# Kernel tuning notes

Hardware: AMD Instinct MI355X
Metric: run time of the kernel (lower is better)

The kernel has to match this reference:

```python
import jax, jax.numpy as jnp
import numpy as np

D_MODEL = 768
NUM_HEADS = 12
D_HEAD = D_MODEL // NUM_HEADS


def setup_inputs() -> dict:
    key = jax.random.key(0)
    ks = jax.random.split(key, 11)
    B, S = 2, 2048
    scale = 1.0 / np.sqrt(D_MODEL)
    inp = {
        "query": jax.random.normal(ks[0], (B, S, D_MODEL), dtype=jnp.float32),
        "key": jax.random.normal(ks[1], (B, S, D_MODEL), dtype=jnp.float32),
        "value": jax.random.normal(ks[2], (B, S, D_MODEL), dtype=jnp.float32),
        "W_q": jax.random.normal(ks[3], (D_MODEL, D_MODEL), dtype=jnp.float32) * scale,
        "b_q": jnp.zeros((D_MODEL,), dtype=jnp.float32),
        "W_k": jax.random.normal(ks[4], (D_MODEL, D_MODEL), dtype=jnp.float32) * scale,
        "b_k": jnp.zeros((D_MODEL,), dtype=jnp.float32),
        "W_v": jax.random.normal(ks[5], (D_MODEL, D_MODEL), dtype=jnp.float32) * scale,
        "b_v": jnp.zeros((D_MODEL,), dtype=jnp.float32),
        "W_o": jax.random.normal(ks[6], (D_MODEL, D_MODEL), dtype=jnp.float32) * scale,
        "b_o": jnp.zeros((D_MODEL,), dtype=jnp.float32),
    }
    return inp


def _split_heads(x):
    # [B, S, D] -> [B, H, S, Dh]
    B, S, _ = x.shape
    return x.reshape(B, S, NUM_HEADS, D_HEAD).transpose(0, 2, 1, 3)


def reference(query, key, value, W_q, b_q, W_k, b_k, W_v, b_v, W_o, b_o):
    q = _split_heads(query @ W_q.T + b_q)   # [B,H,S,Dh]
    k = _split_heads(key @ W_k.T + b_k)
    v = _split_heads(value @ W_v.T + b_v)
    scores = jnp.einsum('bhqd,bhkd->bhqk', q, k) / np.sqrt(D_HEAD).astype(np.float32)
    attn = jax.nn.softmax(scores, axis=-1)  # [B,H,S,S]
    out = jnp.einsum('bhqk,bhkd->bhqd', attn, v)
    B, H, S, Dh = out.shape
    out = out.transpose(0, 2, 1, 3).reshape(B, S, D_MODEL)
    out = out @ W_o.T + b_o
    return out, attn
```

## Files before the change

### kernel.cpp

```cpp
#include <hip/hip_runtime.h>
#include <hip/hip_bf16.h>
#include <stdint.h>

#define B_ 2
#define S_ 2048
#define D_ 768
#define H_ 12
#define DH_ 64
#define M_ (B_ * S_)

typedef __hip_bfloat16 bf16_t;
typedef __attribute__((ext_vector_type(8))) short bf16x8;
typedef __attribute__((ext_vector_type(4))) float f32x4;

__device__ __forceinline__ void async_cp16(const void* g, void* lds) {
  __builtin_amdgcn_global_load_lds(
      (__attribute__((address_space(1))) void*)g,
      (__attribute__((address_space(3))) void*)lds, 16, 0, 0);
}

__global__ __launch_bounds__(256) void cvt_kernel(
    const float* __restrict__ s0, const float* __restrict__ s1,
    const float* __restrict__ s2, const float* __restrict__ s3,
    const float* __restrict__ s4, const float* __restrict__ s5,
    const float* __restrict__ s6,
    bf16_t* __restrict__ d0, bf16_t* __restrict__ d1, bf16_t* __restrict__ d2,
    bf16_t* __restrict__ d3, bf16_t* __restrict__ d4, bf16_t* __restrict__ d5,
    bf16_t* __restrict__ d6) {
  const int NX = 786432;
  const int NW = 147456;
  int idx = blockIdx.x * 256 + threadIdx.x;
  const float* s; bf16_t* d; int l;
  if      (idx < NX)            { s = s0; d = d0; l = idx; }
  else if (idx < 2 * NX)        { s = s1; d = d1; l = idx - NX; }
  else if (idx < 3 * NX)        { s = s2; d = d2; l = idx - 2 * NX; }
  else if (idx < 3 * NX + NW)   { s = s3; d = d3; l = idx - 3 * NX; }
  else if (idx < 3 * NX + 2*NW) { s = s4; d = d4; l = idx - (3 * NX + NW); }
  else if (idx < 3 * NX + 3*NW) { s = s5; d = d5; l = idx - (3 * NX + 2 * NW); }
  else                          { s = s6; d = d6; l = idx - (3 * NX + 3 * NW); }
  float4 f = ((const float4*)s)[l];
  union { bf16_t h[4]; uint64_t u; } pk;
  pk.h[0] = __float2bfloat16(f.x); pk.h[1] = __float2bfloat16(f.y);
  pk.h[2] = __float2bfloat16(f.z); pk.h[3] = __float2bfloat16(f.w);
  ((uint64_t*)d)[l] = pk.u;
}

__device__ __forceinline__ void gemm_core(
    const bf16_t* __restrict__ A, const bf16_t* __restrict__ W,
    bf16_t* sA, bf16_t* sB, int m0, int n0, f32x4 acc[4][4]) {
  const int tid = threadIdx.x;
  const int wave = tid >> 6, lane = tid & 63;
  const int quad = lane >> 4, col = lane & 15;
  const int wm = wave >> 1, wn = wave & 1;

  for (int kt = 0; kt < 768; kt += 64) {
    __syncthreads();
#pragma unroll
    for (int r2 = 0; r2 < 4; ++r2) {
      int cbase = r2 * 256 + wave * 64;
      int c = cbase + lane;
      int row = c >> 3, cpos = c & 7, csrc = cpos ^ (row & 7);
      async_cp16(A + (size_t)(m0 + row) * 768 + kt + csrc * 8, (char*)sA + cbase * 16);
      async_cp16(W + (size_t)(n0 + row) * 768 + kt + csrc * 8, (char*)sB + cbase * 16);
    }
    __syncthreads();
#pragma unroll
    for (int ks = 0; ks < 2; ++ks) {
      const int cl = ks * 4 + quad;
      bf16x8 af[4], bf8[4];
#pragma unroll
      for (int i = 0; i < 4; ++i) {
        int m = wm * 64 + i * 16 + col;
        af[i] = *(const bf16x8*)((const char*)sA + m * 128 + ((cl ^ (m & 7)) * 16));
      }
#pragma unroll
      for (int j = 0; j < 4; ++j) {
        int n = wn * 64 + j * 16 + col;
        bf8[j] = *(const bf16x8*)((const char*)sB + n * 128 + ((cl ^ (n & 7)) * 16));
      }
#pragma unroll
      for (int i = 0; i < 4; ++i)
#pragma unroll
        for (int j = 0; j < 4; ++j)
          acc[i][j] = __builtin_amdgcn_mfma_f32_16x16x32_bf16(af[i], bf8[j], acc[i][j], 0, 0, 0);
    }
  }
}

__global__ __launch_bounds__(256, 2) void qkv_gemm_kernel(
    const bf16_t* __restrict__ xq, const bf16_t* __restrict__ xk, const bf16_t* __restrict__ xv,
    const bf16_t* __restrict__ wq, const bf16_t* __restrict__ wk, const bf16_t* __restrict__ wv,
    const float* __restrict__ bq, const float* __restrict__ bk, const float* __restrict__ bv,
    bf16_t* __restrict__ Qb, bf16_t* __restrict__ Kb, bf16_t* __restrict__ Vt) {
  __shared__ bf16_t sA[128 * 64];
  __shared__ bf16_t sB[128 * 64];
  const int z = blockIdx.z;
  const bf16_t* A = (z == 0) ? xq : (z == 1) ? xk : xv;
  const bf16_t* W = (z == 0) ? wq : (z == 1) ? wk : wv;
  const float* bias = (z == 0) ? bq : (z == 1) ? bk : bv;
  const int m0 = blockIdx.y * 128, n0 = blockIdx.x * 128;
  f32x4 acc[4][4] = {};
  gemm_core(A, W, sA, sB, m0, n0, acc);

  const int tid = threadIdx.x;
  const int wave = tid >> 6, lane = tid & 63;
  const int quad = lane >> 4, col = lane & 15;
  const int wm = wave >> 1, wn = wave & 1;
  float bv4[4];
#pragma unroll
  for (int j = 0; j < 4; ++j) bv4[j] = bias[n0 + wn * 64 + j * 16 + col];

  if (z == 2) {
#pragma unroll
    for (int i = 0; i < 4; ++i)
#pragma unroll
      for (int j = 0; j < 4; ++j) {
        union { bf16_t h[4]; uint64_t u; } pk;
#pragma unroll
        for (int r = 0; r < 4; ++r) pk.h[r] = __float2bfloat16(acc[i][j][r] + bv4[j]);
        int sbase = m0 + wm * 64 + i * 16 + quad * 4;
        int b = sbase >> 11, s = sbase & 2047;
        int ng = n0 + wn * 64 + j * 16 + col;
        int h = ng >> 6, d = ng & 63;
        *(uint64_t*)(Vt + (((size_t)(b * H_ + h)) * DH_ + d) * S_ + s) = pk.u;
      }
  } else {
    const float scale = (z == 0) ? 0.125f : 1.0f;
    bf16_t* dst = (z == 0) ? Qb : Kb;
#pragma unroll
    for (int i = 0; i < 4; ++i)
#pragma unroll
      for (int j = 0; j < 4; ++j)
#pragma unroll
        for (int r = 0; r < 4; ++r) {
          int mg = m0 + wm * 64 + i * 16 + quad * 4 + r;
          int ng = n0 + wn * 64 + j * 16 + col;
          int b = mg >> 11, s = mg & 2047;
          int h = ng >> 6, d = ng & 63;
          dst[(((size_t)(b * H_ + h)) * S_ + s) * DH_ + d] =
              __float2bfloat16((acc[i][j][r] + bv4[j]) * scale);
        }
  }
}

__global__ __launch_bounds__(256, 2) void o_gemm_kernel(
    const bf16_t* __restrict__ Ob, const bf16_t* __restrict__ wo,
    const float* __restrict__ bo, float* __restrict__ out) {
  __shared__ bf16_t sA[128 * 64];
  __shared__ bf16_t sB[128 * 64];
  const int m0 = blockIdx.y * 128, n0 = blockIdx.x * 128;
  f32x4 acc[4][4] = {};
  gemm_core(Ob, wo, sA, sB, m0, n0, acc);
  const int tid = threadIdx.x;
  const int wave = tid >> 6, lane = tid & 63;
  const int quad = lane >> 4, col = lane & 15;
  const int wm = wave >> 1, wn = wave & 1;
  float bv4[4];
#pragma unroll
  for (int j = 0; j < 4; ++j) bv4[j] = bo[n0 + wn * 64 + j * 16 + col];
#pragma unroll
  for (int i = 0; i < 4; ++i)
#pragma unroll
    for (int j = 0; j < 4; ++j)
#pragma unroll
      for (int r = 0; r < 4; ++r) {
        int mg = m0 + wm * 64 + i * 16 + quad * 4 + r;
        int ng = n0 + wn * 64 + j * 16 + col;
        out[(size_t)mg * D_ + ng] = acc[i][j][r] + bv4[j];
      }
}

__global__ __launch_bounds__(256, 3) void attn_kernel(
    const bf16_t* __restrict__ Qb, const bf16_t* __restrict__ Kb,
    const bf16_t* __restrict__ Vt, float* __restrict__ attn,
    bf16_t* __restrict__ Ob) {
  __shared__ bf16_t sP[2][64 * 128];
  __shared__ float red[4][64];

  const int tid = threadIdx.x;
  const int w = tid >> 6, lane = tid & 63;
  const int quad = lane >> 4, col = lane & 15;
  const int qt = blockIdx.x, bh = blockIdx.y;
  const int bb = bh / H_, hh = bh - bb * H_;
  const size_t headSD = (size_t)bh * (S_ * DH_);
  const size_t headDS = (size_t)bh * (DH_ * S_);
  const int q0 = qt * 64;

  bf16x8 aq[2][4];
#pragma unroll
  for (int ks = 0; ks < 2; ++ks)
#pragma unroll
    for (int i = 0; i < 4; ++i)
      aq[ks][i] = *(const bf16x8*)(Qb + headSD +
                    (size_t)(q0 + i * 16 + col) * DH_ + ks * 32 + quad * 8);

  float rsum[4][4] = {};
  for (int t = 0; t < 16; ++t) {
    const int k0 = t * 128 + w * 32;
    bf16x8 bk[2][2];
#pragma unroll
    for (int ks = 0; ks < 2; ++ks)
#pragma unroll
      for (int j = 0; j < 2; ++j)
        bk[ks][j] = *(const bf16x8*)(Kb + headSD +
                      (size_t)(k0 + j * 16 + col) * DH_ + ks * 32 + quad * 8);
    f32x4 sc[4][2] = {};
#pragma unroll
    for (int ks = 0; ks < 2; ++ks)
#pragma unroll
      for (int i = 0; i < 4; ++i)
#pragma unroll
        for (int j = 0; j < 2; ++j)
          sc[i][j] = __builtin_amdgcn_mfma_f32_16x16x32_bf16(aq[ks][i], bk[ks][j], sc[i][j], 0, 0, 0);
#pragma unroll
    for (int i = 0; i < 4; ++i)
#pragma unroll
      for (int r = 0; r < 4; ++r)
        rsum[i][r] += __expf(sc[i][0][r]) + __expf(sc[i][1][r]);
  }
#pragma unroll
  for (int d = 1; d < 16; d <<= 1)
#pragma unroll
    for (int i = 0; i < 4; ++i)
#pragma unroll
      for (int r = 0; r < 4; ++r)
        rsum[i][r] += __shfl_xor(rsum[i][r], d, 64);
  if (col == 0) {
#pragma unroll
    for (int i = 0; i < 4; ++i)
#pragma unroll
      for (int r = 0; r < 4; ++r)
        red[w][i * 16 + quad * 4 + r] = rsum[i][r];
  }
  __syncthreads();
  float li[4][4];
#pragma unroll
  for (int i = 0; i < 4; ++i)
#pragma unroll
    for (int r = 0; r < 4; ++r) {
      int q = i * 16 + quad * 4 + r;
      li[i][r] = 1.0f / (red[0][q] + red[1][q] + red[2][q] + red[3][q]);
    }

  f32x4 oacc[4] = {};
  for (int t = 0; t < 16; ++t) {
    const int k0 = t * 128 + w * 32;
    bf16x8 bk[2][2];
#pragma unroll
    for (int ks = 0; ks < 2; ++ks)
#pragma unroll
      for (int j = 0; j < 2; ++j)
        bk[ks][j] = *(const bf16x8*)(Kb + headSD +
                      (size_t)(k0 + j * 16 + col) * DH_ + ks * 32 + quad * 8);
    f32x4 sc[4][2] = {};
#pragma unroll
    for (int ks = 0; ks < 2; ++ks)
#pragma unroll
      for (int i = 0; i < 4; ++i)
#pragma unroll
        for (int j = 0; j < 2; ++j)
          sc[i][j] = __builtin_amdgcn_mfma_f32_16x16x32_bf16(aq[ks][i], bk[ks][j], sc[i][j], 0, 0, 0);

    bf16_t* P = sP[t & 1];
#pragma unroll
    for (int i = 0; i < 4; ++i)
#pragma unroll
      for (int r = 0; r < 4; ++r) {
        int q = i * 16 + quad * 4 + r;
        float l = li[i][r];
        float* ap = attn + ((size_t)bh * S_ + (q0 + q)) * S_ + t * 128 + w * 32;
#pragma unroll
        for (int j = 0; j < 2; ++j) {
          float pa = __expf(sc[i][j][r]) * l;
          ap[j * 16 + col] = pa;
          int kk = w * 32 + j * 16 + col;
          int sch = (kk >> 3) ^ (q & 15);
          P[q * 128 + sch * 8 + (kk & 7)] = __float2bfloat16(pa);
        }
      }
    __syncthreads();
#pragma unroll
    for (int ksl = 0; ksl < 4; ++ksl) {
      int m = w * 16 + col;
      int sch = (ksl * 4 + quad) ^ (m & 15);
      bf16x8 ap8 = *(const bf16x8*)(P + m * 128 + sch * 8);
      bf16x8 bv[4];
#pragma unroll
      for (int j = 0; j < 4; ++j)
        bv[j] = *(const bf16x8*)(Vt + headDS + (size_t)(col + 16 * j) * S_ +
                                 t * 128 + ksl * 32 + quad * 8);
#pragma unroll
      for (int j = 0; j < 4; ++j)
        oacc[j] = __builtin_amdgcn_mfma_f32_16x16x32_bf16(ap8, bv[j], oacc[j], 0, 0, 0);
    }
  }

#pragma unroll
  for (int j = 0; j < 4; ++j)
#pragma unroll
    for (int r = 0; r < 4; ++r) {
      int q = q0 + w * 16 + quad * 4 + r;
      Ob[((size_t)bb * S_ + q) * D_ + hh * 64 + j * 16 + col] =
          __float2bfloat16(oacc[j][r]);
    }
}

extern "C" void kernel_launch(void* const* d_in, const int* in_sizes, int n_in,
                              void* d_out, int out_size, void* d_ws, size_t ws_size,
                              hipStream_t stream) {
  const float* q  = (const float*)d_in[0];
  const float* k  = (const float*)d_in[1];
  const float* v  = (const float*)d_in[2];
  const float* Wq = (const float*)d_in[3];
  const float* bq = (const float*)d_in[4];
  const float* Wk = (const float*)d_in[5];
  const float* bk = (const float*)d_in[6];
  const float* Wv = (const float*)d_in[7];
  const float* bv = (const float*)d_in[8];
  const float* Wo = (const float*)d_in[9];
  const float* bo = (const float*)d_in[10];
  char* ws = (char*)d_ws;
  bf16_t* xq = (bf16_t*)(ws + 0);
  bf16_t* xk = (bf16_t*)(ws + 6291456);
  bf16_t* xv = (bf16_t*)(ws + 12582912);
  bf16_t* wq = (bf16_t*)(ws + 18874368);
  bf16_t* wk = (bf16_t*)(ws + 20054016);
  bf16_t* wv = (bf16_t*)(ws + 21233664);
  bf16_t* wo = (bf16_t*)(ws + 22413312);
  bf16_t* Qb = (bf16_t*)(ws + 23592960);
  bf16_t* Kb = (bf16_t*)(ws + 29884416);
  bf16_t* Vt = (bf16_t*)(ws + 36175872);
  bf16_t* Ob = (bf16_t*)(ws + 42467328);
  float* out = (float*)d_out;
  float* attn = out + (size_t)M_ * D_;

  cvt_kernel<<<11520, 256, 0, stream>>>(q, k, v, Wq, Wk, Wv, Wo,
                                        xq, xk, xv, wq, wk, wv, wo);
  qkv_gemm_kernel<<<dim3(6, 32, 3), 256, 0, stream>>>(xq, xk, xv, wq, wk, wv,
                                                      bq, bk, bv, Qb, Kb, Vt);
  attn_kernel<<<dim3(32, 24), 256, 0, stream>>>(Qb, Kb, Vt, attn, Ob);
  o_gemm_kernel<<<dim3(6, 32), 256, 0, stream>>>(Ob, wo, bo, out);
}
```

Baseline: 618.1 us.

## Restructure attention so each wave owns 16 query rows, dropping LDS and barriers

Each wave now handles its own 16 query rows across all 2048 keys, where before the four waves split the key range of a 64-row tile. The QK^T product is computed transposed (K as the A operand), so each lane holds four consecutive key columns and the attention matrix is written as float4 vectors. The P fragment for the PV MFMA is rebuilt through cross-lane shuffles rather than an LDS staging buffer, which removes the shared memory, the row-sum reduction through LDS and all __syncthreads. The cost is that every wave now loads the full K and V streams for its head independently (more global/L2 traffic per block), and a loop of 64 short iterations replaces 16 longer ones.

```diff
diff --git a/kernel.cpp b/kernel.cpp
--- a/kernel.cpp
+++ b/kernel.cpp
@@ -174,9 +174,6 @@
     const bf16_t* __restrict__ Qb, const bf16_t* __restrict__ Kb,
     const bf16_t* __restrict__ Vt, float* __restrict__ attn,
     bf16_t* __restrict__ Ob) {
-  __shared__ bf16_t sP[2][64 * 128];
-  __shared__ float red[4][64];
-
   const int tid = threadIdx.x;
   const int w = tid >> 6, lane = tid & 63;
   const int quad = lane >> 4, col = lane & 15;
@@ -184,125 +181,112 @@
   const int bb = bh / H_, hh = bh - bb * H_;
   const size_t headSD = (size_t)bh * (S_ * DH_);
   const size_t headDS = (size_t)bh * (DH_ * S_);
-  const int q0 = qt * 64;
-
-  bf16x8 aq[2][4];
+  const int q0 = qt * 64 + w * 16;
+
+  bf16x8 aq[2];
 #pragma unroll
   for (int ks = 0; ks < 2; ++ks)
-#pragma unroll
-    for (int i = 0; i < 4; ++i)
-      aq[ks][i] = *(const bf16x8*)(Qb + headSD +
-                    (size_t)(q0 + i * 16 + col) * DH_ + ks * 32 + quad * 8);
-
-  float rsum[4][4] = {};
-  for (int t = 0; t < 16; ++t) {
-    const int k0 = t * 128 + w * 32;
+    aq[ks] = *(const bf16x8*)(Qb + headSD +
+                  (size_t)(q0 + col) * DH_ + ks * 32 + quad * 8);
+
+  float rsum = 0.f;
+  for (int t = 0; t < 64; ++t) {
+    const int kg = t * 32;
     bf16x8 bk[2][2];
 #pragma unroll
-    for (int ks = 0; ks < 2; ++ks)
-#pragma unroll
-      for (int j = 0; j < 2; ++j)
-        bk[ks][j] = *(const bf16x8*)(Kb + headSD +
-                      (size_t)(k0 + j * 16 + col) * DH_ + ks * 32 + quad * 8);
-    f32x4 sc[4][2] = {};
-#pragma unroll
-    for (int ks = 0; ks < 2; ++ks)
-#pragma unroll
-      for (int i = 0; i < 4; ++i)
-#pragma unroll
-        for (int j = 0; j < 2; ++j)
-          sc[i][j] = __builtin_amdgcn_mfma_f32_16x16x32_bf16(aq[ks][i], bk[ks][j], sc[i][j], 0, 0, 0);
-#pragma unroll
-    for (int i = 0; i < 4; ++i)
+    for (int kk = 0; kk < 2; ++kk)
+#pragma unroll
+      for (int ks = 0; ks < 2; ++ks)
+        bk[kk][ks] = *(const bf16x8*)(Kb + headSD +
+                        (size_t)(kg + kk * 16 + col) * DH_ + ks * 32 + quad * 8);
+    f32x4 sc[2] = {};
+#pragma unroll
+    for (int kk = 0; kk < 2; ++kk)
+#pragma unroll
+      for (int ks = 0; ks < 2; ++ks)
+        sc[kk] = __builtin_amdgcn_mfma_f32_16x16x32_bf16(bk[kk][ks], aq[ks], sc[kk], 0, 0, 0);
+#pragma unroll
+    for (int kk = 0; kk < 2; ++kk)
 #pragma unroll
       for (int r = 0; r < 4; ++r)
-        rsum[i][r] += __expf(sc[i][0][r]) + __expf(sc[i][1][r]);
+        rsum += __expf(sc[kk][r]);
   }
-#pragma unroll
-  for (int d = 1; d < 16; d <<= 1)
-#pragma unroll
-    for (int i = 0; i < 4; ++i)
+  rsum += __shfl_xor(rsum, 16, 64);
+  rsum += __shfl_xor(rsum, 32, 64);
+  const float li = 1.0f / rsum;
+
+  f32x4 oacc[4] = {};
+  float* aprow = attn + ((size_t)bh * S_ + (q0 + col)) * S_ + quad * 4;
+  for (int t = 0; t < 64; ++t) {
+    const int kg = t * 32;
+    bf16x8 bk[2][2];
+#pragma unroll
+    for (int kk = 0; kk < 2; ++kk)
+#pragma unroll
+      for (int ks = 0; ks < 2; ++ks)
+        bk[kk][ks] = *(const bf16x8*)(Kb + headSD +
+                        (size_t)(kg + kk * 16 + col) * DH_ + ks * 32 + quad * 8);
+    f32x4 sc[2] = {};
+#pragma unroll
+    for (int kk = 0; kk < 2; ++kk)
+#pragma unroll
+      for (int ks = 0; ks < 2; ++ks)
+        sc[kk] = __builtin_amdgcn_mfma_f32_16x16x32_bf16(bk[kk][ks], aq[ks], sc[kk], 0, 0, 0);
+
+    float pa[2][4];
+#pragma unroll
+    for (int kk = 0; kk < 2; ++kk)
 #pragma unroll
       for (int r = 0; r < 4; ++r)
-        rsum[i][r] += __shfl_xor(rsum[i][r], d, 64);
-  if (col == 0) {
-#pragma unroll
-    for (int i = 0; i < 4; ++i)
-#pragma unroll
-      for (int r = 0; r < 4; ++r)
-        red[w][i * 16 + quad * 4 + r] = rsum[i][r];
+        pa[kk][r] = __expf(sc[kk][r]) * li;
+
+    *(f32x4*)(aprow + kg)      = (f32x4){pa[0][0], pa[0][1], pa[0][2], pa[0][3]};
+    *(f32x4*)(aprow + kg + 16) = (f32x4){pa[1][0], pa[1][1], pa[1][2], pa[1][3]};
+
+    uint32_t dw[2][2];
+#pragma unroll
+    for (int kk = 0; kk < 2; ++kk)
+#pragma unroll
+      for (int p = 0; p < 2; ++p) {
+        union { bf16_t h[2]; uint32_t u; } pk2;
+        pk2.h[0] = __float2bfloat16(pa[kk][2 * p]);
+        pk2.h[1] = __float2bfloat16(pa[kk][2 * p + 1]);
+        dw[kk][p] = pk2.u;
+      }
+
+    const int s0 = ((2 * quad) & 3) * 16 + col;
+    const int s1 = ((2 * quad + 1) & 3) * 16 + col;
+    uint32_t a00 = (uint32_t)__shfl((int)dw[0][0], s0);
+    uint32_t a01 = (uint32_t)__shfl((int)dw[0][1], s0);
+    uint32_t a10 = (uint32_t)__shfl((int)dw[1][0], s0);
+    uint32_t a11 = (uint32_t)__shfl((int)dw[1][1], s0);
+    uint32_t b00 = (uint32_t)__shfl((int)dw[0][0], s1);
+    uint32_t b01 = (uint32_t)__shfl((int)dw[0][1], s1);
+    uint32_t b10 = (uint32_t)__shfl((int)dw[1][0], s1);
+    uint32_t b11 = (uint32_t)__shfl((int)dw[1][1], s1);
+    const bool hi2 = quad >= 2;
+    union { uint32_t u[4]; bf16x8 v; } fr;
+    fr.u[0] = hi2 ? a10 : a00;
+    fr.u[1] = hi2 ? a11 : a01;
+    fr.u[2] = hi2 ? b10 : b00;
+    fr.u[3] = hi2 ? b11 : b01;
+
+    bf16x8 bv[4];
+#pragma unroll
+    for (int j = 0; j < 4; ++j)
+      bv[j] = *(const bf16x8*)(Vt + headDS +
+                  (size_t)(16 * j + col) * S_ + kg + quad * 8);
+#pragma unroll
+    for (int j = 0; j < 4; ++j)
+      oacc[j] = __builtin_amdgcn_mfma_f32_16x16x32_bf16(fr.v, bv[j], oacc[j], 0, 0, 0);
   }
-  __syncthreads();
-  float li[4][4];
-#pragma unroll
-  for (int i = 0; i < 4; ++i)
-#pragma unroll
-    for (int r = 0; r < 4; ++r) {
-      int q = i * 16 + quad * 4 + r;
-      li[i][r] = 1.0f / (red[0][q] + red[1][q] + red[2][q] + red[3][q]);
-    }
-
-  f32x4 oacc[4] = {};
-  for (int t = 0; t < 16; ++t) {
-    const int k0 = t * 128 + w * 32;
-    bf16x8 bk[2][2];
-#pragma unroll
-    for (int ks = 0; ks < 2; ++ks)
-#pragma unroll
-      for (int j = 0; j < 2; ++j)
-        bk[ks][j] = *(const bf16x8*)(Kb + headSD +
-                      (size_t)(k0 + j * 16 + col) * DH_ + ks * 32 + quad * 8);
-    f32x4 sc[4][2] = {};
-#pragma unroll
-    for (int ks = 0; ks < 2; ++ks)
-#pragma unroll
-      for (int i = 0; i < 4; ++i)
-#pragma unroll
-        for (int j = 0; j < 2; ++j)
-          sc[i][j] = __builtin_amdgcn_mfma_f32_16x16x32_bf16(aq[ks][i], bk[ks][j], sc[i][j], 0, 0, 0);
-
-    bf16_t* P = sP[t & 1];
-#pragma unroll
-    for (int i = 0; i < 4; ++i)
-#pragma unroll
-      for (int r = 0; r < 4; ++r) {
-        int q = i * 16 + quad * 4 + r;
-        float l = li[i][r];
-        float* ap = attn + ((size_t)bh * S_ + (q0 + q)) * S_ + t * 128 + w * 32;
-#pragma unroll
-        for (int j = 0; j < 2; ++j) {
-          float pa = __expf(sc[i][j][r]) * l;
-          ap[j * 16 + col] = pa;
-          int kk = w * 32 + j * 16 + col;
-          int sch = (kk >> 3) ^ (q & 15);
-          P[q * 128 + sch * 8 + (kk & 7)] = __float2bfloat16(pa);
-        }
-      }
-    __syncthreads();
-#pragma unroll
-    for (int ksl = 0; ksl < 4; ++ksl) {
-      int m = w * 16 + col;
-      int sch = (ksl * 4 + quad) ^ (m & 15);
-      bf16x8 ap8 = *(const bf16x8*)(P + m * 128 + sch * 8);
-      bf16x8 bv[4];
-#pragma unroll
-      for (int j = 0; j < 4; ++j)
-        bv[j] = *(const bf16x8*)(Vt + headDS + (size_t)(col + 16 * j) * S_ +
-                                 t * 128 + ksl * 32 + quad * 8);
-#pragma unroll
-      for (int j = 0; j < 4; ++j)
-        oacc[j] = __builtin_amdgcn_mfma_f32_16x16x32_bf16(ap8, bv[j], oacc[j], 0, 0, 0);
-    }
-  }
 
 #pragma unroll
   for (int j = 0; j < 4; ++j)
 #pragma unroll
-    for (int r = 0; r < 4; ++r) {
-      int q = q0 + w * 16 + quad * 4 + r;
-      Ob[((size_t)bb * S_ + q) * D_ + hh * 64 + j * 16 + col] =
+    for (int r = 0; r < 4; ++r)
+      Ob[((size_t)bb * S_ + (q0 + quad * 4 + r)) * D_ + hh * 64 + 16 * j + col] =
           __float2bfloat16(oacc[j][r]);
-    }
 }
 
 extern "C" void kernel_launch(void* const* d_in, const int* in_sizes, int n_in,
```

Result: slower. 727.8 us (+17.7%).
